# Optimization experiments

Hardware: AMD Instinct MI355X
Metric: run time of the kernel (lower is better)

## Reference

```python
import jax, jax.numpy as jnp
import numpy as np

B, S, D, H = 4, 2048, 1024, 16
HD = D // H

def setup_inputs() -> dict:
    key = jax.random.key(0)
    ks = jax.random.split(key, 9)
    sc = 0.02
    return {
        "x": jax.random.normal(ks[0], (B, S, D), dtype=jnp.float32),
        "Wq": jax.random.normal(ks[1], (D, D), dtype=jnp.float32) * sc,
        "bq": jax.random.normal(ks[2], (D,), dtype=jnp.float32) * sc,
        "Wk": jax.random.normal(ks[3], (D, D), dtype=jnp.float32) * sc,
        "bk": jax.random.normal(ks[4], (D,), dtype=jnp.float32) * sc,
        "Wv": jax.random.normal(ks[5], (D, D), dtype=jnp.float32) * sc,
        "bv": jax.random.normal(ks[6], (D,), dtype=jnp.float32) * sc,
        "Wo": jax.random.normal(ks[7], (D, D), dtype=jnp.float32) * sc,
        "bo": jax.random.normal(ks[8], (D,), dtype=jnp.float32) * sc,
    }

def reference(x, Wq, bq, Wk, bk, Wv, bv, Wo, bo):
    b, n, d = x.shape
    # projections, split heads: [b, h, n, hd]
    def split_heads(t):
        return t.reshape(b, n, H, HD).transpose(0, 2, 1, 3)
    q = split_heads(x @ Wq.T + bq)
    k = split_heads(x @ Wk.T + bk)
    v = split_heads(x @ Wv.T + bv)
    # scores [b, h, n, n], causal mask (triu above diagonal -> -inf)
    scores = jnp.einsum("bhqd,bhkd->bhqk", q, k)
    causal = jnp.tril(jnp.ones((n, n), dtype=bool))  # True = keep
    scores = jnp.where(causal, scores, -jnp.inf)
    # note: module divides by sqrt(head_dim) AFTER masking, same result
    attn = jax.nn.softmax(scores / jnp.sqrt(jnp.float32(HD)), axis=-1)
    ctx = jnp.einsum("bhqk,bhkd->bhqd", attn, v)
    ctx = ctx.transpose(0, 2, 1, 3).reshape(b, n, d)
    return ctx @ Wo.T + bo
```

## Files before the change

kernel.cpp:

```cpp
#include <hip/hip_runtime.h>
#include <stdint.h>

#define BATCH 4
#define S_LEN 2048
#define D_DIM 1024
#define NH 16
#define HD 64
#define M_ROWS (BATCH * S_LEN)
#define NQB (S_LEN / 128)
#define QSCALE 0.18033688011f

using u16 = unsigned short;
typedef __attribute__((ext_vector_type(8))) __bf16 bf16x8;
typedef __attribute__((ext_vector_type(4))) float f32x4;
typedef __attribute__((ext_vector_type(16))) float f32x16;
typedef __attribute__((ext_vector_type(8))) unsigned short u16x8;

__device__ __forceinline__ float exp2fast(float x) { return __builtin_amdgcn_exp2f(x); }

__device__ __forceinline__ u16 f2bf(float f) {
  unsigned u = __builtin_bit_cast(unsigned, f);
  u += 0x7fffu + ((u >> 16) & 1u);
  return (u16)(u >> 16);
}
__device__ __forceinline__ unsigned pk2(float lo, float hi) {
  return __builtin_amdgcn_perm(__builtin_bit_cast(unsigned, hi),
                               __builtin_bit_cast(unsigned, lo), 0x07060302u);
}

__global__ void cvt_bf16_kernel(const float* __restrict__ in, u16* __restrict__ out, int n4) {
  int i = blockIdx.x * blockDim.x + threadIdx.x;
  if (i < n4) {
    float4 v = ((const float4*)in)[i];
    ushort4 o;
    o.x = f2bf(v.x); o.y = f2bf(v.y); o.z = f2bf(v.z); o.w = f2bf(v.w);
    ((ushort4*)out)[i] = o;
  }
}

__global__ void cvt_w_kernel(const float* __restrict__ W0, const float* __restrict__ W1,
                             const float* __restrict__ W2, const float* __restrict__ W3,
                             u16* __restrict__ out) {
  int y = blockIdx.y;
  const float* src = (y == 0) ? W0 : (y == 1) ? W1 : (y == 2) ? W2 : W3;
  u16* dst = out + (size_t)y * D_DIM * D_DIM;
  int i = blockIdx.x * blockDim.x + threadIdx.x;
  float4 v = ((const float4*)src)[i];
  ushort4 o;
  o.x = f2bf(v.x); o.y = f2bf(v.y); o.z = f2bf(v.z); o.w = f2bf(v.w);
  ((ushort4*)dst)[i] = o;
}

__device__ __forceinline__ void stage_tile(const u16* __restrict__ src, int srcK,
                                           u16* dst, int w, int lane) {
#pragma unroll
  for (int i = 0; i < 4; ++i) {
    int ic = w * 4 + i;
    int c = ic * 64 + lane;
    int row = c >> 3, g = c & 7, gs = g ^ (row & 7);
    __builtin_amdgcn_global_load_lds(
        (const __attribute__((address_space(1))) void*)(src + (size_t)row * srcK + gs * 8),
        (__attribute__((address_space(3))) void*)(dst + ic * 512), 16, 0, 0);
  }
}

__global__ __launch_bounds__(256)
void gemm_qkv_kernel(const u16* __restrict__ A, const u16* __restrict__ Bt,
                     const float* __restrict__ bq, const float* __restrict__ bk,
                     const float* __restrict__ bv,
                     u16* __restrict__ Qo, u16* __restrict__ Ko, u16* __restrict__ Vo) {
  __shared__ __align__(16) u16 As[128 * 64];
  __shared__ __align__(16) u16 Bs[128 * 64];
  const int tid = threadIdx.x;
  const int w = tid >> 6;
  const int lane = tid & 63;
  const int l15 = lane & 15, l4 = lane >> 4;
  const int m0 = blockIdx.y * 128, n0 = blockIdx.x * 128;
  const int wr = (w >> 1) * 64, wc = (w & 1) * 64;
  const int K = D_DIM;

  f32x4 acc[4][4] = {};

  for (int k0 = 0; k0 < K; k0 += 64) {
    __syncthreads();
    stage_tile(A + (size_t)m0 * K + k0, K, As, w, lane);
    stage_tile(Bt + (size_t)n0 * K + k0, K, Bs, w, lane);
    __syncthreads();

    bf16x8 a[4][2];
#pragma unroll
    for (int mb = 0; mb < 4; ++mb) {
#pragma unroll
      for (int ks = 0; ks < 2; ++ks) {
        int row = wr + mb * 16 + l15;
        int gsw = (ks * 4 + l4) ^ (row & 7);
        a[mb][ks] = *(const bf16x8*)(As + row * 64 + gsw * 8);
      }
    }
#pragma unroll
    for (int nb = 0; nb < 4; ++nb) {
      int row = wc + nb * 16 + l15;
      int g0 = (0 + l4) ^ (row & 7);
      int g1 = (4 + l4) ^ (row & 7);
      bf16x8 b0 = *(const bf16x8*)(Bs + row * 64 + g0 * 8);
      bf16x8 b1 = *(const bf16x8*)(Bs + row * 64 + g1 * 8);
#pragma unroll
      for (int mb = 0; mb < 4; ++mb) {
        acc[mb][nb] = __builtin_amdgcn_mfma_f32_16x16x32_bf16(a[mb][0], b0, acc[mb][nb], 0, 0, 0);
        acc[mb][nb] = __builtin_amdgcn_mfma_f32_16x16x32_bf16(a[mb][1], b1, acc[mb][nb], 0, 0, 0);
      }
    }
  }

  const int which = n0 >> 10;
  const float* bias = (which == 0) ? bq : (which == 1) ? bk : bv;
  u16* dst = (which == 0) ? Qo : (which == 1) ? Ko : Vo;
  const float scale = (which == 0) ? QSCALE : 1.0f;

#pragma unroll
  for (int mb = 0; mb < 4; ++mb) {
#pragma unroll
    for (int nb = 0; nb < 4; ++nb) {
#pragma unroll
      for (int r = 0; r < 4; ++r) {
        int m = m0 + wr + mb * 16 + l4 * 4 + r;
        int n = n0 + wc + nb * 16 + l15;
        int col = n & 1023;
        float v = (acc[mb][nb][r] + bias[col]) * scale;
        int bb = m >> 11;
        int ss = m & (S_LEN - 1);
        int hh = col >> 6;
        int hd = col & (HD - 1);
        dst[(((size_t)bb * NH + hh) * S_LEN + ss) * HD + hd] = f2bf(v);
      }
    }
  }
}

__global__ __launch_bounds__(256)
void gemm_out_kernel(const u16* __restrict__ A, const u16* __restrict__ Bt,
                     const float* __restrict__ bias, float* __restrict__ Cout) {
  __shared__ __align__(16) u16 As[128 * 64];
  __shared__ __align__(16) u16 Bs[128 * 64];
  const int tid = threadIdx.x;
  const int w = tid >> 6;
  const int lane = tid & 63;
  const int l15 = lane & 15, l4 = lane >> 4;
  const int m0 = blockIdx.y * 128, n0 = blockIdx.x * 128;
  const int wr = (w >> 1) * 64, wc = (w & 1) * 64;
  const int K = D_DIM, N = D_DIM;

  f32x4 acc[4][4] = {};

  for (int k0 = 0; k0 < K; k0 += 64) {
    __syncthreads();
    stage_tile(A + (size_t)m0 * K + k0, K, As, w, lane);
    stage_tile(Bt + (size_t)n0 * K + k0, K, Bs, w, lane);
    __syncthreads();

    bf16x8 a[4][2];
#pragma unroll
    for (int mb = 0; mb < 4; ++mb) {
#pragma unroll
      for (int ks = 0; ks < 2; ++ks) {
        int row = wr + mb * 16 + l15;
        int gsw = (ks * 4 + l4) ^ (row & 7);
        a[mb][ks] = *(const bf16x8*)(As + row * 64 + gsw * 8);
      }
    }
#pragma unroll
    for (int nb = 0; nb < 4; ++nb) {
      int row = wc + nb * 16 + l15;
      int g0 = (0 + l4) ^ (row & 7);
      int g1 = (4 + l4) ^ (row & 7);
      bf16x8 b0 = *(const bf16x8*)(Bs + row * 64 + g0 * 8);
      bf16x8 b1 = *(const bf16x8*)(Bs + row * 64 + g1 * 8);
#pragma unroll
      for (int mb = 0; mb < 4; ++mb) {
        acc[mb][nb] = __builtin_amdgcn_mfma_f32_16x16x32_bf16(a[mb][0], b0, acc[mb][nb], 0, 0, 0);
        acc[mb][nb] = __builtin_amdgcn_mfma_f32_16x16x32_bf16(a[mb][1], b1, acc[mb][nb], 0, 0, 0);
      }
    }
  }

#pragma unroll
  for (int mb = 0; mb < 4; ++mb) {
#pragma unroll
    for (int nb = 0; nb < 4; ++nb) {
#pragma unroll
      for (int r = 0; r < 4; ++r) {
        int m = m0 + wr + mb * 16 + l4 * 4 + r;
        int n = n0 + wc + nb * 16 + l15;
        Cout[(size_t)m * N + n] = acc[mb][nb][r] + bias[n];
      }
    }
  }
}

__device__ __forceinline__ void stage_k(const u16* __restrict__ Kg, size_t base, int kt,
                                        u16* Kd, int w, int lane) {
#pragma unroll
  for (int i = 0; i < 2; ++i) {
    int ic = w * 2 + i;
    int c = ic * 64 + lane;
    int row = c >> 3, g = c & 7, gs = g ^ (row & 7);
    __builtin_amdgcn_global_load_lds(
        (const __attribute__((address_space(1))) void*)(Kg + base + (size_t)(kt * 64 + row) * HD + gs * 8),
        (__attribute__((address_space(3))) void*)(Kd + ic * 512), 16, 0, 0);
  }
}

__device__ __forceinline__ void pfrag(const f32x16& st, int hi, bf16x8& fa, bf16x8& fb) {
  unsigned c0 = pk2(st[0], st[1]),   c1 = pk2(st[2], st[3]);
  unsigned c2 = pk2(st[4], st[5]),   c3 = pk2(st[6], st[7]);
  unsigned c4 = pk2(st[8], st[9]),   c5 = pk2(st[10], st[11]);
  unsigned c6 = pk2(st[12], st[13]), c7 = pk2(st[14], st[15]);
  unsigned p0 = __shfl_xor(c0, 32), p1 = __shfl_xor(c1, 32);
  unsigned p2 = __shfl_xor(c2, 32), p3 = __shfl_xor(c3, 32);
  unsigned p4 = __shfl_xor(c4, 32), p5 = __shfl_xor(c5, 32);
  unsigned p6 = __shfl_xor(c6, 32), p7 = __shfl_xor(c7, 32);
  union { unsigned u[4]; bf16x8 v; } a, b;
  a.u[0] = hi ? p2 : c0; a.u[1] = hi ? p3 : c1;
  a.u[2] = hi ? c2 : p0; a.u[3] = hi ? c3 : p1;
  b.u[0] = hi ? p6 : c4; b.u[1] = hi ? p7 : c5;
  b.u[2] = hi ? c6 : p4; b.u[3] = hi ? c7 : p5;
  fa = a.v; fb = b.v;
}

__global__ __launch_bounds__(256)
void attn_kernel(const u16* __restrict__ Q, const u16* __restrict__ Kg,
                 const u16* __restrict__ Vg, u16* __restrict__ ctx) {
  __shared__ __align__(16) u16 Ks[2][64 * 64];
  __shared__ __align__(16) u16 Vt[64 * 64];

  const int tid = threadIdx.x;
  const int w = tid >> 6, lane = tid & 63;
  const int l31 = lane & 31, hi = lane >> 5;
  const int hi4 = hi * 4, hi8 = hi * 8;
  const int bh = blockIdx.y;
  const size_t base = (size_t)bh * S_LEN * HD;
  const int b = bh >> 4, h = bh & (NH - 1);

  const int vkey = tid & 63;
  const int vd0 = (tid >> 6) * 16;

#pragma unroll 1
  for (int seg = 0; seg < 2; ++seg) {
    const int qb = seg ? (NQB - 1 - blockIdx.x) : blockIdx.x;
    const int Qw = qb * 128 + w * 32;
    const int q_g = Qw + l31;

    bf16x8 qf[4];
#pragma unroll
    for (int step = 0; step < 4; ++step)
      qf[step] = *(const bf16x8*)(Q + base + (size_t)q_g * HD + step * 16 + hi8);

    f32x16 oacc0 = {}, oacc1 = {};
    float mrun = -1e30f, lrun = 0.f;

    const int nkt = 2 * qb + 2;

    stage_k(Kg, base, 0, Ks[0], w, lane);
    u16x8 vv0, vv1;
    {
      const u16* gv = Vg + base + (size_t)vkey * HD + vd0;
      vv0 = *(const u16x8*)gv;
      vv1 = *(const u16x8*)(gv + 8);
    }

    for (int kt = 0; kt < nkt; ++kt) {
      const int cur = kt & 1;
      const bool more = (kt + 1 < nkt);

#pragma unroll
      for (int j = 0; j < 8; ++j) {
        int d0 = vd0 + j;
        Vt[d0 * 64 + (((vkey >> 3) ^ ((d0 >> 2) & 7)) << 3) + (vkey & 7)] = vv0[j];
        int d1 = vd0 + 8 + j;
        Vt[d1 * 64 + (((vkey >> 3) ^ ((d1 >> 2) & 7)) << 3) + (vkey & 7)] = vv1[j];
      }
      __syncthreads();

      if (more) {
        stage_k(Kg, base, kt + 1, Ks[cur ^ 1], w, lane);
        const u16* gv = Vg + base + (size_t)((kt + 1) * 64 + vkey) * HD + vd0;
        vv0 = *(const u16x8*)gv;
        vv1 = *(const u16x8*)(gv + 8);
      }

      const u16* Kb = &Ks[cur][0];

      if (kt * 64 <= Qw + 31) {
        f32x16 st0 = {}, st1 = {};
#pragma unroll
        for (int step = 0; step < 4; ++step) {
          int r0 = l31, r1 = 32 + l31;
          bf16x8 kf0 = *(const bf16x8*)(Kb + r0 * 64 + (((step * 2 + hi) ^ (r0 & 7)) << 3));
          bf16x8 kf1 = *(const bf16x8*)(Kb + r1 * 64 + (((step * 2 + hi) ^ (r1 & 7)) << 3));
          st0 = __builtin_amdgcn_mfma_f32_32x32x16_bf16(kf0, qf[step], st0, 0, 0, 0);
          st1 = __builtin_amdgcn_mfma_f32_32x32x16_bf16(kf1, qf[step], st1, 0, 0, 0);
        }

        if (kt * 64 + 63 > Qw) {
#pragma unroll
          for (int r = 0; r < 16; ++r) {
            int key0 = kt * 64 + hi4 + (r & 3) + 8 * (r >> 2);
            if (key0 > q_g) st0[r] = -1e30f;
            if (key0 + 32 > q_g) st1[r] = -1e30f;
          }
        }

        float mt[16];
#pragma unroll
        for (int r = 0; r < 16; ++r) mt[r] = fmaxf(st0[r], st1[r]);
#pragma unroll
        for (int s = 8; s >= 1; s >>= 1)
#pragma unroll
          for (int r = 0; r < 8; ++r)
            if (r < s) mt[r] = fmaxf(mt[r], mt[r + s]);
        float tm = fmaxf(mt[0], __shfl_xor(mt[0], 32));

        if (__any(tm > mrun)) {
          float mnew = fmaxf(mrun, tm);
          float rs = exp2fast(mrun - mnew);
          mrun = mnew;
          lrun *= rs;
#pragma unroll
          for (int r = 0; r < 16; ++r) {
            float rsb = __shfl(rs, (r & 3) + 8 * (r >> 2) + hi4);
            oacc0[r] *= rsb;
            oacc1[r] *= rsb;
          }
        }

        float sa[16];
#pragma unroll
        for (int r = 0; r < 16; ++r) {
          st0[r] = exp2fast(st0[r] - mrun);
          st1[r] = exp2fast(st1[r] - mrun);
          sa[r] = st0[r] + st1[r];
        }
#pragma unroll
        for (int s = 8; s >= 1; s >>= 1)
#pragma unroll
          for (int r = 0; r < 8; ++r)
            if (r < s) sa[r] += sa[r + s];
        lrun += sa[0] + __shfl_xor(sa[0], 32);

        bf16x8 paf0, paf1, paf2, paf3;
        pfrag(st0, hi, paf0, paf1);
        pfrag(st1, hi, paf2, paf3);

#pragma unroll
        for (int ks = 0; ks < 4; ++ks) {
          bf16x8 pa = (ks == 0) ? paf0 : (ks == 1) ? paf1 : (ks == 2) ? paf2 : paf3;
          int d0 = l31;
          bf16x8 vf0 = *(const bf16x8*)(Vt + d0 * 64 + (((ks * 2 + hi) ^ ((d0 >> 2) & 7)) << 3));
          int d1 = 32 + l31;
          bf16x8 vf1 = *(const bf16x8*)(Vt + d1 * 64 + (((ks * 2 + hi) ^ ((d1 >> 2) & 7)) << 3));
          oacc0 = __builtin_amdgcn_mfma_f32_32x32x16_bf16(pa, vf0, oacc0, 0, 0, 0);
          oacc1 = __builtin_amdgcn_mfma_f32_32x32x16_bf16(pa, vf1, oacc1, 0, 0, 0);
        }
      }
      __syncthreads();
    }

#pragma unroll
    for (int r = 0; r < 16; ++r) {
      float lr = __shfl(lrun, (r & 3) + 8 * (r >> 2) + hi4);
      float inv = 1.0f / lr;
      int srow = Qw + (r & 3) + 8 * (r >> 2) + hi4;
      size_t rowbase = ((size_t)b * S_LEN + srow) * D_DIM + h * HD;
      ctx[rowbase + l31] = f2bf(oacc0[r] * inv);
      ctx[rowbase + 32 + l31] = f2bf(oacc1[r] * inv);
    }
  }
}

extern "C" void kernel_launch(void* const* d_in, const int* in_sizes, int n_in,
                              void* d_out, int out_size, void* d_ws, size_t ws_size,
                              hipStream_t stream) {
  const float* x  = (const float*)d_in[0];
  const float* Wq = (const float*)d_in[1];
  const float* bq = (const float*)d_in[2];
  const float* Wk = (const float*)d_in[3];
  const float* bk = (const float*)d_in[4];
  const float* Wv = (const float*)d_in[5];
  const float* bv = (const float*)d_in[6];
  const float* Wo = (const float*)d_in[7];
  const float* bo = (const float*)d_in[8];

  char* ws = (char*)d_ws;
  const size_t MB = 1024 * 1024;
  u16* xb     = (u16*)(ws + 0);
  u16* Wqkvb  = (u16*)(ws + 16 * MB);
  u16* Wob    = (u16*)(ws + 22 * MB);
  u16* Qb     = (u16*)(ws + 24 * MB);
  u16* Kb     = (u16*)(ws + 40 * MB);
  u16* Vb     = (u16*)(ws + 56 * MB);
  u16* ctxb   = xb;

  cvt_bf16_kernel<<<(M_ROWS * D_DIM / 4 + 255) / 256, 256, 0, stream>>>(x, xb, M_ROWS * D_DIM / 4);
  cvt_w_kernel<<<dim3(D_DIM * D_DIM / 4 / 256, 4), 256, 0, stream>>>(Wq, Wk, Wv, Wo, Wqkvb);

  gemm_qkv_kernel<<<dim3(3 * D_DIM / 128, M_ROWS / 128), 256, 0, stream>>>(
      xb, Wqkvb, bq, bk, bv, Qb, Kb, Vb);

  attn_kernel<<<dim3(NQB / 2, BATCH * NH), 256, 0, stream>>>(Qb, Kb, Vb, ctxb);

  gemm_out_kernel<<<dim3(D_DIM / 128, M_ROWS / 128), 256, 0, stream>>>(
      ctxb, Wob, bo, (float*)d_out);
}
```

Measured before the change: 196.3 us.

## Read K fragments directly from global and double-buffer transposed V in LDS

Drops LDS staging of K tiles: each lane now loads its K fragments straight from global memory (L2/L1) instead of through global_load_lds into a swizzled buffer. V is double-buffered in LDS so that the next tile's transpose-store overlaps with the current tile's compute, leaving one barrier per iteration. MFMA sections are wrapped in s_setprio to favour issue. The trade-off is more direct global traffic and latency for K, with less LDS usage and fewer barriers.

New measurement: 286.6 us. 46.0% more time.

```diff
diff --git a/kernel.cpp b/kernel.cpp
--- a/kernel.cpp
+++ b/kernel.cpp
@@ -194,19 +194,6 @@
         Cout[(size_t)m * N + n] = acc[mb][nb][r] + bias[n];
       }
     }
-  }
-}
-
-__device__ __forceinline__ void stage_k(const u16* __restrict__ Kg, size_t base, int kt,
-                                        u16* Kd, int w, int lane) {
-#pragma unroll
-  for (int i = 0; i < 2; ++i) {
-    int ic = w * 2 + i;
-    int c = ic * 64 + lane;
-    int row = c >> 3, g = c & 7, gs = g ^ (row & 7);
-    __builtin_amdgcn_global_load_lds(
-        (const __attribute__((address_space(1))) void*)(Kg + base + (size_t)(kt * 64 + row) * HD + gs * 8),
-        (__attribute__((address_space(3))) void*)(Kd + ic * 512), 16, 0, 0);
   }
 }
 
@@ -230,8 +217,7 @@
 __global__ __launch_bounds__(256)
 void attn_kernel(const u16* __restrict__ Q, const u16* __restrict__ Kg,
                  const u16* __restrict__ Vg, u16* __restrict__ ctx) {
-  __shared__ __align__(16) u16 Ks[2][64 * 64];
-  __shared__ __align__(16) u16 Vt[64 * 64];
+  __shared__ __align__(16) u16 Vt[2][64 * 64];
 
   const int tid = threadIdx.x;
   const int w = tid >> 6, lane = tid & 63;
@@ -260,46 +246,56 @@
 
     const int nkt = 2 * qb + 2;
 
-    stage_k(Kg, base, 0, Ks[0], w, lane);
     u16x8 vv0, vv1;
     {
       const u16* gv = Vg + base + (size_t)vkey * HD + vd0;
       vv0 = *(const u16x8*)gv;
       vv1 = *(const u16x8*)(gv + 8);
-    }
+#pragma unroll
+      for (int j = 0; j < 8; ++j) {
+        int d0 = vd0 + j, d1 = vd0 + 8 + j;
+        Vt[0][d0 * 64 + (((vkey >> 3) ^ ((d0 >> 2) & 7)) << 3) + (vkey & 7)] = vv0[j];
+        Vt[0][d1 * 64 + (((vkey >> 3) ^ ((d1 >> 2) & 7)) << 3) + (vkey & 7)] = vv1[j];
+      }
+      if (nkt > 1) {
+        const u16* gv1 = Vg + base + (size_t)(64 + vkey) * HD + vd0;
+        vv0 = *(const u16x8*)gv1;
+        vv1 = *(const u16x8*)(gv1 + 8);
+      }
+    }
+    __syncthreads();
 
     for (int kt = 0; kt < nkt; ++kt) {
       const int cur = kt & 1;
-      const bool more = (kt + 1 < nkt);
-
-#pragma unroll
-      for (int j = 0; j < 8; ++j) {
-        int d0 = vd0 + j;
-        Vt[d0 * 64 + (((vkey >> 3) ^ ((d0 >> 2) & 7)) << 3) + (vkey & 7)] = vv0[j];
-        int d1 = vd0 + 8 + j;
-        Vt[d1 * 64 + (((vkey >> 3) ^ ((d1 >> 2) & 7)) << 3) + (vkey & 7)] = vv1[j];
-      }
-      __syncthreads();
-
-      if (more) {
-        stage_k(Kg, base, kt + 1, Ks[cur ^ 1], w, lane);
-        const u16* gv = Vg + base + (size_t)((kt + 1) * 64 + vkey) * HD + vd0;
-        vv0 = *(const u16x8*)gv;
-        vv1 = *(const u16x8*)(gv + 8);
-      }
-
-      const u16* Kb = &Ks[cur][0];
+
+      if (kt + 1 < nkt) {
+#pragma unroll
+        for (int j = 0; j < 8; ++j) {
+          int d0 = vd0 + j, d1 = vd0 + 8 + j;
+          Vt[cur ^ 1][d0 * 64 + (((vkey >> 3) ^ ((d0 >> 2) & 7)) << 3) + (vkey & 7)] = vv0[j];
+          Vt[cur ^ 1][d1 * 64 + (((vkey >> 3) ^ ((d1 >> 2) & 7)) << 3) + (vkey & 7)] = vv1[j];
+        }
+        if (kt + 2 < nkt) {
+          const u16* gv = Vg + base + (size_t)((kt + 2) * 64 + vkey) * HD + vd0;
+          vv0 = *(const u16x8*)gv;
+          vv1 = *(const u16x8*)(gv + 8);
+        }
+      }
 
       if (kt * 64 <= Qw + 31) {
+        const u16* Krow0 = Kg + base + (size_t)(kt * 64 + l31) * HD;
+        const u16* Krow1 = Kg + base + (size_t)(kt * 64 + 32 + l31) * HD;
+
         f32x16 st0 = {}, st1 = {};
+        __builtin_amdgcn_s_setprio(1);
 #pragma unroll
         for (int step = 0; step < 4; ++step) {
-          int r0 = l31, r1 = 32 + l31;
-          bf16x8 kf0 = *(const bf16x8*)(Kb + r0 * 64 + (((step * 2 + hi) ^ (r0 & 7)) << 3));
-          bf16x8 kf1 = *(const bf16x8*)(Kb + r1 * 64 + (((step * 2 + hi) ^ (r1 & 7)) << 3));
+          bf16x8 kf0 = *(const bf16x8*)(Krow0 + step * 16 + hi8);
+          bf16x8 kf1 = *(const bf16x8*)(Krow1 + step * 16 + hi8);
           st0 = __builtin_amdgcn_mfma_f32_32x32x16_bf16(kf0, qf[step], st0, 0, 0, 0);
           st1 = __builtin_amdgcn_mfma_f32_32x32x16_bf16(kf1, qf[step], st1, 0, 0, 0);
         }
+        __builtin_amdgcn_s_setprio(0);
 
         if (kt * 64 + 63 > Qw) {
 #pragma unroll
@@ -351,16 +347,19 @@
         pfrag(st0, hi, paf0, paf1);
         pfrag(st1, hi, paf2, paf3);
 
+        const u16* Vb = &Vt[cur][0];
+        __builtin_amdgcn_s_setprio(1);
 #pragma unroll
         for (int ks = 0; ks < 4; ++ks) {
           bf16x8 pa = (ks == 0) ? paf0 : (ks == 1) ? paf1 : (ks == 2) ? paf2 : paf3;
           int d0 = l31;
-          bf16x8 vf0 = *(const bf16x8*)(Vt + d0 * 64 + (((ks * 2 + hi) ^ ((d0 >> 2) & 7)) << 3));
+          bf16x8 vf0 = *(const bf16x8*)(Vb + d0 * 64 + (((ks * 2 + hi) ^ ((d0 >> 2) & 7)) << 3));
           int d1 = 32 + l31;
-          bf16x8 vf1 = *(const bf16x8*)(Vt + d1 * 64 + (((ks * 2 + hi) ^ ((d1 >> 2) & 7)) << 3));
+          bf16x8 vf1 = *(const bf16x8*)(Vb + d1 * 64 + (((ks * 2 + hi) ^ ((d1 >> 2) & 7)) << 3));
           oacc0 = __builtin_amdgcn_mfma_f32_32x32x16_bf16(pa, vf0, oacc0, 0, 0, 0);
           oacc1 = __builtin_amdgcn_mfma_f32_32x32x16_bf16(pa, vf1, oacc1, 0, 0, 0);
         }
+        __builtin_amdgcn_s_setprio(0);
       }
       __syncthreads();
     }
@@ -374,6 +373,7 @@
       ctx[rowbase + l31] = f2bf(oacc0[r] * inv);
       ctx[rowbase + 32 + l31] = f2bf(oacc1[r] * inv);
     }
+    __syncthreads();
   }
 }
 
```

## Split attention KV range across two wave groups and merge softmax partials in LDS

Applied to the files above, without the earlier changes.

Doubles the attention block to 512 threads. Two groups of four waves each process half of the key tiles for the same 128-query block, with separate K/V LDS buffers. The partial outputs and running max/sum are then combined through LDS in a flash-decoding style merge. The aim is to raise per-block parallelism and occupancy on the causal loop, since the grid is only 8x64 blocks. The cost is more LDS, an extra merge step with a barrier, and load imbalance, because the masked diagonal tiles all fall in the second group.

After: 259.7 us. 32.3% more time.

```diff
diff --git a/kernel.cpp b/kernel.cpp
--- a/kernel.cpp
+++ b/kernel.cpp
@@ -198,10 +198,10 @@
 }
 
 __device__ __forceinline__ void stage_k(const u16* __restrict__ Kg, size_t base, int kt,
-                                        u16* Kd, int w, int lane) {
+                                        u16* Kd, int wg, int lane) {
 #pragma unroll
   for (int i = 0; i < 2; ++i) {
-    int ic = w * 2 + i;
+    int ic = wg * 2 + i;
     int c = ic * 64 + lane;
     int row = c >> 3, g = c & 7, gs = g ^ (row & 7);
     __builtin_amdgcn_global_load_lds(
@@ -227,27 +227,28 @@
   fa = a.v; fb = b.v;
 }
 
-__global__ __launch_bounds__(256)
+__global__ __launch_bounds__(512, 4)
 void attn_kernel(const u16* __restrict__ Q, const u16* __restrict__ Kg,
                  const u16* __restrict__ Vg, u16* __restrict__ ctx) {
-  __shared__ __align__(16) u16 Ks[2][64 * 64];
-  __shared__ __align__(16) u16 Vt[64 * 64];
+  __shared__ __align__(16) u16 Ks[2][2][64 * 64];
+  __shared__ __align__(16) u16 Vt[2][64 * 64];
 
   const int tid = threadIdx.x;
   const int w = tid >> 6, lane = tid & 63;
+  const int grp = w >> 2, wg = w & 3;
   const int l31 = lane & 31, hi = lane >> 5;
   const int hi4 = hi * 4, hi8 = hi * 8;
   const int bh = blockIdx.y;
   const size_t base = (size_t)bh * S_LEN * HD;
   const int b = bh >> 4, h = bh & (NH - 1);
 
-  const int vkey = tid & 63;
-  const int vd0 = (tid >> 6) * 16;
+  const int vkey = lane;
+  const int vd0 = wg * 16;
 
 #pragma unroll 1
   for (int seg = 0; seg < 2; ++seg) {
     const int qb = seg ? (NQB - 1 - blockIdx.x) : blockIdx.x;
-    const int Qw = qb * 128 + w * 32;
+    const int Qw = qb * 128 + wg * 32;
     const int q_g = Qw + l31;
 
     bf16x8 qf[4];
@@ -258,37 +259,39 @@
     f32x16 oacc0 = {}, oacc1 = {};
     float mrun = -1e30f, lrun = 0.f;
 
-    const int nkt = 2 * qb + 2;
-
-    stage_k(Kg, base, 0, Ks[0], w, lane);
+    const int nkt2 = qb + 1;
+    const int kt0 = grp * nkt2;
+
+    stage_k(Kg, base, kt0, Ks[grp][0], wg, lane);
     u16x8 vv0, vv1;
     {
-      const u16* gv = Vg + base + (size_t)vkey * HD + vd0;
+      const u16* gv = Vg + base + (size_t)(kt0 * 64 + vkey) * HD + vd0;
       vv0 = *(const u16x8*)gv;
       vv1 = *(const u16x8*)(gv + 8);
     }
 
-    for (int kt = 0; kt < nkt; ++kt) {
-      const int cur = kt & 1;
-      const bool more = (kt + 1 < nkt);
+    for (int it = 0; it < nkt2; ++it) {
+      const int kt = kt0 + it;
+      const int cur = it & 1;
+      const bool more = (it + 1 < nkt2);
 
 #pragma unroll
       for (int j = 0; j < 8; ++j) {
         int d0 = vd0 + j;
-        Vt[d0 * 64 + (((vkey >> 3) ^ ((d0 >> 2) & 7)) << 3) + (vkey & 7)] = vv0[j];
+        Vt[grp][d0 * 64 + (((vkey >> 3) ^ ((d0 >> 2) & 7)) << 3) + (vkey & 7)] = vv0[j];
         int d1 = vd0 + 8 + j;
-        Vt[d1 * 64 + (((vkey >> 3) ^ ((d1 >> 2) & 7)) << 3) + (vkey & 7)] = vv1[j];
+        Vt[grp][d1 * 64 + (((vkey >> 3) ^ ((d1 >> 2) & 7)) << 3) + (vkey & 7)] = vv1[j];
       }
       __syncthreads();
 
       if (more) {
-        stage_k(Kg, base, kt + 1, Ks[cur ^ 1], w, lane);
+        stage_k(Kg, base, kt + 1, Ks[grp][cur ^ 1], wg, lane);
         const u16* gv = Vg + base + (size_t)((kt + 1) * 64 + vkey) * HD + vd0;
         vv0 = *(const u16x8*)gv;
         vv1 = *(const u16x8*)(gv + 8);
       }
 
-      const u16* Kb = &Ks[cur][0];
+      const u16* Kb = &Ks[grp][cur][0];
 
       if (kt * 64 <= Qw + 31) {
         f32x16 st0 = {}, st1 = {};
@@ -355,9 +358,9 @@
         for (int ks = 0; ks < 4; ++ks) {
           bf16x8 pa = (ks == 0) ? paf0 : (ks == 1) ? paf1 : (ks == 2) ? paf2 : paf3;
           int d0 = l31;
-          bf16x8 vf0 = *(const bf16x8*)(Vt + d0 * 64 + (((ks * 2 + hi) ^ ((d0 >> 2) & 7)) << 3));
+          bf16x8 vf0 = *(const bf16x8*)(&Vt[grp][0] + d0 * 64 + (((ks * 2 + hi) ^ ((d0 >> 2) & 7)) << 3));
           int d1 = 32 + l31;
-          bf16x8 vf1 = *(const bf16x8*)(Vt + d1 * 64 + (((ks * 2 + hi) ^ ((d1 >> 2) & 7)) << 3));
+          bf16x8 vf1 = *(const bf16x8*)(&Vt[grp][0] + d1 * 64 + (((ks * 2 + hi) ^ ((d1 >> 2) & 7)) << 3));
           oacc0 = __builtin_amdgcn_mfma_f32_32x32x16_bf16(pa, vf0, oacc0, 0, 0, 0);
           oacc1 = __builtin_amdgcn_mfma_f32_32x32x16_bf16(pa, vf1, oacc1, 0, 0, 0);
         }
@@ -365,14 +368,42 @@
       __syncthreads();
     }
 
-#pragma unroll
-    for (int r = 0; r < 16; ++r) {
-      float lr = __shfl(lrun, (r & 3) + 8 * (r >> 2) + hi4);
-      float inv = 1.0f / lr;
-      int srow = Qw + (r & 3) + 8 * (r >> 2) + hi4;
-      size_t rowbase = ((size_t)b * S_LEN + srow) * D_DIM + h * HD;
-      ctx[rowbase + l31] = f2bf(oacc0[r] * inv);
-      ctx[rowbase + 32 + l31] = f2bf(oacc1[r] * inv);
+    {
+      float* cb = (float*)(&Ks[0][0][0]);
+      float* ml = (float*)(&Vt[0][0]);
+      if (grp == 1) {
+#pragma unroll
+        for (int r = 0; r < 16; ++r) {
+          int row = (r & 3) + 8 * (r >> 2) + hi4;
+          cb[wg * 2048 + row * 64 + l31] = oacc0[r];
+          cb[wg * 2048 + row * 64 + 32 + l31] = oacc1[r];
+        }
+        if (hi == 0) { ml[wg * 32 + l31] = mrun; ml[128 + wg * 32 + l31] = lrun; }
+      }
+      __syncthreads();
+      if (grp == 0) {
+        float m1 = ml[wg * 32 + l31];
+        float l1 = ml[128 + wg * 32 + l31];
+        float M = fmaxf(mrun, m1);
+        float s0 = exp2fast(mrun - M);
+        float s1 = exp2fast(m1 - M);
+        float lsum = lrun * s0 + l1 * s1;
+#pragma unroll
+        for (int r = 0; r < 16; ++r) {
+          int rq = (r & 3) + 8 * (r >> 2) + hi4;
+          float s0b = __shfl(s0, rq);
+          float s1b = __shfl(s1, rq);
+          float lb  = __shfl(lsum, rq);
+          float o0 = oacc0[r] * s0b + cb[wg * 2048 + rq * 64 + l31] * s1b;
+          float o1 = oacc1[r] * s0b + cb[wg * 2048 + rq * 64 + 32 + l31] * s1b;
+          float inv = 1.0f / lb;
+          int srow = Qw + rq;
+          size_t rowbase = ((size_t)b * S_LEN + srow) * D_DIM + h * HD;
+          ctx[rowbase + l31] = f2bf(o0 * inv);
+          ctx[rowbase + 32 + l31] = f2bf(o1 * inv);
+        }
+      }
+      __syncthreads();
     }
   }
 }
@@ -406,7 +437,7 @@
   gemm_qkv_kernel<<<dim3(3 * D_DIM / 128, M_ROWS / 128), 256, 0, stream>>>(
       xb, Wqkvb, bq, bk, bv, Qb, Kb, Vb);
 
-  attn_kernel<<<dim3(NQB / 2, BATCH * NH), 256, 0, stream>>>(Qb, Kb, Vb, ctxb);
+  attn_kernel<<<dim3(NQB / 2, BATCH * NH), 512, 0, stream>>>(Qb, Kb, Vb, ctxb);
 
   gemm_out_kernel<<<dim3(D_DIM / 128, M_ROWS / 128), 256, 0, stream>>>(
       ctxb, Wob, bo, (float*)d_out);
```
